# Optimization experiments

Hardware: AMD Instinct MI355X
Metric: run time of the kernel (lower is better)

The kernel has to match this reference:

```python
import jax, jax.numpy as jnp
import numpy as np
from jax.ops import segment_sum

B = 4096      # graphs per side (= batch of triples)
NPG = 32      # nodes per graph
N = B * NPG   # total nodes per batched graph
EPG = 128     # edges per graph
E = B * EPG   # total edges per batched graph
D = 256       # emb_dim
D4 = D // 4   # gnn1 out dim


def setup_inputs() -> dict:
    key = jax.random.key(0)
    ks = jax.random.split(key, 16)
    base = jnp.repeat(jnp.arange(B, dtype=jnp.int32) * NPG, EPG)  # graph offsets per edge
    def edges(k1, k2):
        s = base + jax.random.randint(k1, (E,), 0, NPG, dtype=jnp.int32)
        d = base + jax.random.randint(k2, (E,), 0, NPG, dtype=jnp.int32)
        return s, d
    subj_src, subj_dst = edges(ks[0], ks[1])
    obj_src, obj_dst = edges(ks[2], ks[3])
    node_graph_ids = jnp.repeat(jnp.arange(B, dtype=jnp.int32), NPG)
    # negative sampling indices (precomputed randomness, as in _sample_batch_negative_triples)
    head_or_tail = jax.random.randint(ks[4], (B,), 0, 2, dtype=jnp.int32)
    random_rows = jax.random.permutation(ks[5], B).astype(jnp.int32)
    ar = jnp.arange(B, dtype=jnp.int32)
    corrupt_hidx = jnp.where(head_or_tail == 1, random_rows, ar)
    corrupt_tidx = jnp.where(head_or_tail == 0, random_rows, ar)
    s = 0.02
    p = lambda k, sh: jax.random.normal(k, sh, dtype=jnp.float32) * s
    return {
        "subj_node_embs": jax.random.normal(ks[6], (N, D), dtype=jnp.float32),
        "obj_node_embs": jax.random.normal(ks[7], (N, D), dtype=jnp.float32),
        "rel_tok_embs": jax.random.normal(ks[8], (B, D), dtype=jnp.float32),
        "subj_src": subj_src, "subj_dst": subj_dst,
        "obj_src": obj_src, "obj_dst": obj_dst,
        "node_graph_ids": node_graph_ids,
        "corrupt_hidx": corrupt_hidx, "corrupt_tidx": corrupt_tidx,
        "WO1": p(ks[9], (D4, D)), "bO1": jnp.zeros((D4,), jnp.float32),
        "WI1": p(ks[10], (D4, D)), "bI1": jnp.zeros((D4,), jnp.float32),
        "WO2": p(ks[11], (D, D4)), "bO2": jnp.zeros((D,), jnp.float32),
        "WI2": p(ks[12], (D, D4)), "bI2": jnp.zeros((D,), jnp.float32),
        "relW": p(ks[13], (D, D)), "relb": jnp.zeros((D,), jnp.float32),
    }


def _mean_agg(h, idx_from, idx_to, n):
    # mean over edges (idx_from -> idx_to) of h[idx_from], per destination node; 0 for isolated
    deg = segment_sum(jnp.ones((idx_from.shape[0],), h.dtype), idx_to, num_segments=n)
    s = segment_sum(jnp.take(h, idx_from, axis=0), idx_to, num_segments=n)
    return s / jnp.maximum(deg, 1.0)[:, None]


def _compgcn(src, dst, h, WO, bO, WI, bI):
    n = h.shape[0]
    ho = _mean_agg(h, src, dst, n)   # forward graph: mean of in-neighbor sources
    hi = _mean_agg(h, dst, src, n)   # reversed graph: mean of out-neighbor targets
    return (ho @ WO.T + bO) + (hi @ WI.T + bI)


def _graph_emb(src, dst, node_embs, gids, WO1, bO1, WI1, bI1, WO2, bO2, WI2, bI2):
    hn = jax.nn.relu(_compgcn(src, dst, node_embs, WO1, bO1, WI1, bI1))
    hn = jax.nn.relu(_compgcn(src, dst, hn, WO2, bO2, WI2, bI2))
    # mean readout per graph
    cnt = segment_sum(jnp.ones((hn.shape[0],), hn.dtype), gids, num_segments=B)
    return segment_sum(hn, gids, num_segments=B) / cnt[:, None]


def _dist(h, r, t):
    return jnp.linalg.norm(h + r - t, ord=2, axis=1)


def reference(subj_node_embs, obj_node_embs, rel_tok_embs,
              subj_src, subj_dst, obj_src, obj_dst, node_graph_ids,
              corrupt_hidx, corrupt_tidx,
              WO1, bO1, WI1, bI1, WO2, bO2, WI2, bI2, relW, relb):
    h_embs = _graph_emb(subj_src, subj_dst, subj_node_embs, node_graph_ids,
                        WO1, bO1, WI1, bI1, WO2, bO2, WI2, bI2)
    t_embs = _graph_emb(obj_src, obj_dst, obj_node_embs, node_graph_ids,
                        WO1, bO1, WI1, bI1, WO2, bO2, WI2, bI2)
    r_embs = jax.nn.relu(rel_tok_embs @ relW.T + relb)
    pos_scores = _dist(h_embs, r_embs, t_embs)
    neg_scores = _dist(h_embs[corrupt_hidx], r_embs, t_embs[corrupt_tidx])
    return pos_scores, neg_scores
```

## Files before the change

kernel.cpp:

```cpp
#include <hip/hip_runtime.h>
#include <hip/hip_bf16.h>

#define BGR 4096
#define DIM 256
#define HS  257

#define OFF_EB 0
#define OFF_H1 0
#define OFF_A2 4608
#define OFF_YT 16896
#define OFF_CW 27136

typedef __bf16 bf16x8 __attribute__((ext_vector_type(8)));
typedef __bf16 bf16x4 __attribute__((ext_vector_type(4)));
typedef float  f32x4  __attribute__((ext_vector_type(4)));

__device__ __forceinline__ unsigned short f2b(float f) {
  unsigned u = __builtin_bit_cast(unsigned, f);
  u = (u + 0x7FFFu + ((u >> 16) & 1u)) >> 16;
  return (unsigned short)u;
}

__device__ __forceinline__ bf16x4 cvt4(f32x4 c) {
  bf16x4 r;
  r[0] = (__bf16)c[0]; r[1] = (__bf16)c[1]; r[2] = (__bf16)c[2]; r[3] = (__bf16)c[3];
  return r;
}

__global__ void wcvt_kernel(
    const float* __restrict__ WO1, const float* __restrict__ WI1,
    const float* __restrict__ WO2, const float* __restrict__ WI2,
    const float* __restrict__ bO1, const float* __restrict__ bI1,
    const float* __restrict__ bO2, const float* __restrict__ bI2,
    unsigned short* __restrict__ W1b, unsigned short* __restrict__ W2b,
    float* __restrict__ b1, float* __restrict__ b2)
{
  const int i = blockIdx.x * 256 + threadIdx.x;
  { int j = i >> 8, k = i & 255;
    float v = (j < 64) ? WO1[j * 256 + k] : WI1[(j - 64) * 256 + k];
    W1b[i] = f2b(v); }
  { int j = i >> 7, k = i & 127;
    float v = (k < 64) ? WO2[j * 64 + k] : WI2[j * 64 + (k - 64)];
    W2b[i] = f2b(v); }
  if (i < 64)  b1[i] = bO1[i] + bI1[i];
  if (i < 256) b2[i] = bO2[i] + bI2[i];
}

__global__ __launch_bounds__(256)
__attribute__((amdgpu_waves_per_eu(1, 5)))
void fused_kernel(
    const float* __restrict__ subj, const float* __restrict__ obj,
    const int* __restrict__ ssrc, const int* __restrict__ sdst,
    const int* __restrict__ osrc, const int* __restrict__ odst,
    const unsigned short* __restrict__ W1b, const unsigned short* __restrict__ W2b,
    const float* __restrict__ b1, const float* __restrict__ b2,
    float* __restrict__ gout)
{
  __shared__ __align__(16) unsigned char S[28416];
  const int t = threadIdx.x, w = t >> 6, l = t & 63;
  const int ln16 = l & 15, kg = l >> 4;
  const int gid = blockIdx.x;
  const int side = gid >> 12, g = gid & (BGR - 1);
  unsigned* cw = (unsigned*)(S + OFF_CW);
  const float* Eg = (side ? obj : subj) + (size_t)g * 32 * DIM;

  float4 ev[8];
  #pragma unroll
  for (int i = 0; i < 8; i++)
    ev[i] = *(const float4*)(Eg + (w * 8 + i) * 256 + l * 4);
  int es = 0, ed = 0;
  if (t < 128) {
    es = (side ? osrc : ssrc)[g * 128 + t] & 31;
    ed = (side ? odst : sdst)[g * 128 + t] & 31;
  }
  for (int i = t; i < 320; i += 256) cw[i] = 0;
  __syncthreads();

  if (t < 128) {
    atomicAdd(&cw[ed * 8 + (es >> 2)], 1u << ((es & 3) * 8));
    atomicAdd(&cw[256 + ed], 1u);
    atomicAdd(&cw[288 + es], 1u);
  }
  #pragma unroll
  for (int i = 0; i < 8; i++) {
    f32x4 tmp = {ev[i].x, ev[i].y, ev[i].z, ev[i].w};
    *(bf16x4*)(S + OFF_EB + (w * 8 + i) * 528 + l * 8) = cvt4(tmp);
  }
  bf16x8 B0[8], B1[8];
  {
    const unsigned short* wb0 = W1b + ((2 * w) * 16 + ln16) * 256 + kg * 8;
    const unsigned short* wb1 = W1b + ((2 * w + 1) * 16 + ln16) * 256 + kg * 8;
    #pragma unroll
    for (int ks = 0; ks < 8; ks++) {
      B0[ks] = *(const bf16x8*)(wb0 + ks * 32);
      B1[ks] = *(const bf16x8*)(wb1 + ks * 32);
    }
  }
  __syncthreads();

  {
    f32x4 a00 = {0,0,0,0}, a01 = {0,0,0,0}, a10 = {0,0,0,0}, a11 = {0,0,0,0};
    const unsigned char* ea = S + OFF_EB + ln16 * 528 + kg * 16;
    #pragma unroll
    for (int ks = 0; ks < 8; ks++) {
      bf16x8 A0 = *(const bf16x8*)(ea + ks * 64);
      bf16x8 A1 = *(const bf16x8*)(ea + 16 * 528 + ks * 64);
      a00 = __builtin_amdgcn_mfma_f32_16x16x32_bf16(A0, B0[ks], a00, 0, 0, 0);
      a01 = __builtin_amdgcn_mfma_f32_16x16x32_bf16(A0, B1[ks], a01, 0, 0, 0);
      a10 = __builtin_amdgcn_mfma_f32_16x16x32_bf16(A1, B0[ks], a10, 0, 0, 0);
      a11 = __builtin_amdgcn_mfma_f32_16x16x32_bf16(A1, B1[ks], a11, 0, 0, 0);
    }
    *(bf16x4*)(S + OFF_YT + ((2 * w) * 16 + ln16) * 80 + (kg * 4) * 2)          = cvt4(a00);
    *(bf16x4*)(S + OFF_YT + ((2 * w + 1) * 16 + ln16) * 80 + (kg * 4) * 2)      = cvt4(a01);
    *(bf16x4*)(S + OFF_YT + ((2 * w) * 16 + ln16) * 80 + (16 + kg * 4) * 2)     = cvt4(a10);
    *(bf16x4*)(S + OFF_YT + ((2 * w + 1) * 16 + ln16) * 80 + (16 + kg * 4) * 2) = cvt4(a11);
  }
  __syncthreads();

  bf16x8 m1f[2], m2f[2];
  #pragma unroll
  for (int hf = 0; hf < 2; hf++) {
    const int r = hf * 16 + ln16;
    const float fi = 1.0f / fmaxf((float)cw[256 + r], 1.0f);
    const float fo = 1.0f / fmaxf((float)cw[288 + r], 1.0f);
    const unsigned w0 = cw[r * 8 + kg * 2], w1 = cw[r * 8 + kg * 2 + 1];
    bf16x8 a, b;
    #pragma unroll
    for (int q = 0; q < 4; q++) {
      a[q]     = (__bf16)((float)((w0 >> (q * 8)) & 255u) * fi);
      a[4 + q] = (__bf16)((float)((w1 >> (q * 8)) & 255u) * fi);
    }
    #pragma unroll
    for (int q = 0; q < 8; q++) {
      const unsigned wq = cw[(kg * 8 + q) * 8 + (r >> 2)];
      b[q] = (__bf16)((float)((wq >> ((r & 3) * 8)) & 255u) * fo);
    }
    m1f[hf] = a; m2f[hf] = b;
  }
  {
    bf16x8 Byo = *(const bf16x8*)(S + OFF_YT + (w * 16 + ln16) * 80 + kg * 16);
    bf16x8 Byi = *(const bf16x8*)(S + OFF_YT + (64 + w * 16 + ln16) * 80 + kg * 16);
    const float b1j = b1[w * 16 + ln16];
    #pragma unroll
    for (int mt = 0; mt < 2; mt++) {
      f32x4 z = {0.f, 0.f, 0.f, 0.f};
      f32x4 c = __builtin_amdgcn_mfma_f32_16x16x32_bf16(m1f[mt], Byo, z, 0, 0, 0);
      c = __builtin_amdgcn_mfma_f32_16x16x32_bf16(m2f[mt], Byi, c, 0, 0, 0);
      f32x4 hv = { fmaxf(c[0] + b1j, 0.f), fmaxf(c[1] + b1j, 0.f),
                   fmaxf(c[2] + b1j, 0.f), fmaxf(c[3] + b1j, 0.f) };
      *(bf16x4*)(S + OFF_H1 + (w * 16 + ln16) * 72 + (mt * 16 + kg * 4) * 2) = cvt4(hv);
    }
  }
  __syncthreads();

  {
    bf16x8 Af = *(const bf16x8*)(S + OFF_H1 + (w * 16 + ln16) * 72 + kg * 16);
    #pragma unroll
    for (int hf = 0; hf < 2; hf++)
      #pragma unroll
      for (int ntd = 0; ntd < 2; ntd++) {
        f32x4 z = {0.f, 0.f, 0.f, 0.f};
        f32x4 c = __builtin_amdgcn_mfma_f32_16x16x32_bf16(
            Af, hf ? m2f[ntd] : m1f[ntd], z, 0, 0, 0);
        *(bf16x4*)(S + OFF_A2 + (ntd * 16 + ln16) * 272 + hf * 128 + w * 32 + kg * 8) = cvt4(c);
      }
  }
  __syncthreads();

  {
    bf16x8 BF[2][4];
    #pragma unroll
    for (int ntd = 0; ntd < 2; ntd++)
      #pragma unroll
      for (int ks = 0; ks < 4; ks++)
        BF[ntd][ks] = *(const bf16x8*)(S + OFF_A2 + (ntd * 16 + ln16) * 272 + ks * 64 + kg * 16);
    #pragma unroll
    for (int q = 0; q < 4; q++) {
      const int mt = w * 4 + q;
      bf16x8 AW[4];
      #pragma unroll
      for (int ks = 0; ks < 4; ks++)
        AW[ks] = *(const bf16x8*)(W2b + (mt * 16 + ln16) * 128 + ks * 32 + kg * 8);
      f32x4 a0 = {0.f, 0.f, 0.f, 0.f}, a1 = {0.f, 0.f, 0.f, 0.f};
      #pragma unroll
      for (int ks = 0; ks < 4; ks++) {
        a0 = __builtin_amdgcn_mfma_f32_16x16x32_bf16(AW[ks], BF[0][ks], a0, 0, 0, 0);
        a1 = __builtin_amdgcn_mfma_f32_16x16x32_bf16(AW[ks], BF[1][ks], a1, 0, 0, 0);
      }
      const float4 bb = *(const float4*)(b2 + mt * 16 + kg * 4);
      float v0 = fmaxf(a0[0] + bb.x, 0.f) + fmaxf(a1[0] + bb.x, 0.f);
      float v1 = fmaxf(a0[1] + bb.y, 0.f) + fmaxf(a1[1] + bb.y, 0.f);
      float v2 = fmaxf(a0[2] + bb.z, 0.f) + fmaxf(a1[2] + bb.z, 0.f);
      float v3 = fmaxf(a0[3] + bb.w, 0.f) + fmaxf(a1[3] + bb.w, 0.f);
      #pragma unroll
      for (int d = 1; d < 16; d <<= 1) {
        v0 += __shfl_xor(v0, d); v1 += __shfl_xor(v1, d);
        v2 += __shfl_xor(v2, d); v3 += __shfl_xor(v3, d);
      }
      if (ln16 == 0) {
        float4 o = { v0 * 0.03125f, v1 * 0.03125f, v2 * 0.03125f, v3 * 0.03125f };
        *(float4*)(gout + (size_t)gid * DIM + mt * 16 + kg * 4) = o;
      }
    }
  }
}

__global__ __launch_bounds__(256, 4) void rel_kernel(
    const float* __restrict__ rel, const float* __restrict__ relW,
    const float* __restrict__ relb, float* __restrict__ r_out)
{
  __shared__ float srel[16 * HS];
  const int t = threadIdx.x;
  const int b0 = blockIdx.x << 4;
  #pragma unroll
  for (int i = 0; i < 4; i++) {
    int f = (i << 8) + t;
    int r = f >> 6, k4 = f & 63;
    float4 x = *(const float4*)(rel + (size_t)(b0 + r) * DIM + (k4 << 2));
    float* d = &srel[r * HS + (k4 << 2)];
    d[0] = x.x; d[1] = x.y; d[2] = x.z; d[3] = x.w;
  }
  __syncthreads();
  const int r = t & 15, jg = t >> 4;
  const float* pa = &srel[r * HS];
  const float* w = relW + (size_t)(jg * 16) * DIM;
  float acc[16];
  #pragma unroll
  for (int jj = 0; jj < 16; jj++) acc[jj] = 0.f;
  for (int k0 = 0; k0 < DIM; k0 += 16) {
    float a[16];
    #pragma unroll
    for (int u = 0; u < 16; u++) a[u] = pa[k0 + u];
    #pragma unroll
    for (int jj = 0; jj < 16; jj++) {
      const float* wr = w + jj * DIM + k0;
      #pragma unroll
      for (int u = 0; u < 16; u += 4) {
        float4 wv = *(const float4*)(wr + u);
        acc[jj] += a[u]*wv.x + a[u+1]*wv.y + a[u+2]*wv.z + a[u+3]*wv.w;
      }
    }
  }
  float* outp = r_out + (size_t)(b0 + r) * DIM + jg * 16;
  #pragma unroll
  for (int jj = 0; jj < 16; jj++) outp[jj] = fmaxf(acc[jj] + relb[jg * 16 + jj], 0.f);
}

__global__ __launch_bounds__(256) void dist_kernel(
    const float* __restrict__ hemb, const float* __restrict__ temb,
    const float* __restrict__ remb, const int* __restrict__ chx,
    const int* __restrict__ ctx, float* __restrict__ out)
{
  const int t = threadIdx.x;
  const int w = t >> 6, l = t & 63;
  const int b = (blockIdx.x << 2) + w;
  float4 h4 = *(const float4*)(hemb + (size_t)b * DIM + (l << 2));
  float4 r4 = *(const float4*)(remb + (size_t)b * DIM + (l << 2));
  float4 t4 = *(const float4*)(temb + (size_t)b * DIM + (l << 2));
  int hb = chx[b], tb = ctx[b];
  float4 hn = *(const float4*)(hemb + (size_t)hb * DIM + (l << 2));
  float4 tn = *(const float4*)(temb + (size_t)tb * DIM + (l << 2));
  float x0 = h4.x + r4.x - t4.x, x1 = h4.y + r4.y - t4.y;
  float x2 = h4.z + r4.z - t4.z, x3 = h4.w + r4.w - t4.w;
  float dp = x0*x0 + x1*x1 + x2*x2 + x3*x3;
  float y0 = hn.x + r4.x - tn.x, y1 = hn.y + r4.y - tn.y;
  float y2 = hn.z + r4.z - tn.z, y3 = hn.w + r4.w - tn.w;
  float dn = y0*y0 + y1*y1 + y2*y2 + y3*y3;
  #pragma unroll
  for (int off = 32; off >= 1; off >>= 1) {
    dp += __shfl_down(dp, off);
    dn += __shfl_down(dn, off);
  }
  if (l == 0) {
    out[b] = sqrtf(dp);
    out[BGR + b] = sqrtf(dn);
  }
}

extern "C" void kernel_launch(void* const* d_in, const int* in_sizes, int n_in,
                              void* d_out, int out_size, void* d_ws, size_t ws_size,
                              hipStream_t stream) {
  const float* subj_embs = (const float*)d_in[0];
  const float* obj_embs  = (const float*)d_in[1];
  const float* rel_tok   = (const float*)d_in[2];
  const int* subj_src = (const int*)d_in[3];
  const int* subj_dst = (const int*)d_in[4];
  const int* obj_src  = (const int*)d_in[5];
  const int* obj_dst  = (const int*)d_in[6];
  const int* chx = (const int*)d_in[8];
  const int* ctx = (const int*)d_in[9];
  const float* WO1 = (const float*)d_in[10];
  const float* bO1 = (const float*)d_in[11];
  const float* WI1 = (const float*)d_in[12];
  const float* bI1 = (const float*)d_in[13];
  const float* WO2 = (const float*)d_in[14];
  const float* bO2 = (const float*)d_in[15];
  const float* WI2 = (const float*)d_in[16];
  const float* bI2 = (const float*)d_in[17];
  const float* relW = (const float*)d_in[18];
  const float* relb = (const float*)d_in[19];

  float* g_embs = (float*)d_ws;
  float* r_embs = g_embs + (size_t)2 * BGR * DIM;
  unsigned short* W1b = (unsigned short*)((char*)d_ws + 12582912);
  unsigned short* W2b = W1b + 32768;
  float* b1 = (float*)((char*)d_ws + 12713984);
  float* b2 = b1 + 64;
  float* out = (float*)d_out;

  wcvt_kernel<<<128, 256, 0, stream>>>(WO1, WI1, WO2, WI2, bO1, bI1, bO2, bI2,
                                       W1b, W2b, b1, b2);
  fused_kernel<<<8192, 256, 0, stream>>>(
      subj_embs, obj_embs, subj_src, subj_dst, obj_src, obj_dst,
      W1b, W2b, b1, b2, g_embs);
  rel_kernel<<<BGR / 16, 256, 0, stream>>>(rel_tok, relW, relb, r_embs);
  dist_kernel<<<BGR / 4, 256, 0, stream>>>(
      g_embs, g_embs + (size_t)BGR * DIM, r_embs, chx, ctx, out);
}
```

Baseline: 208.6 us.

## Process four graphs per block with prefetch of next graph's embeddings and edges

Each block of the fused GNN kernel now loops over four graphs instead of one. The W1 register fragments and bias load are amortized across them, and the next graph's node embeddings and edge indices are prefetched into registers while the current graph computes. Edge-count histograms are double-buffered in shared memory so the next graph's atomics can run mid-pipeline. This cuts the grid to a quarter, which lowers parallelism and lengthens each block's serial chain, and register pressure rises from the prefetched data.

```diff
diff --git a/kernel.cpp b/kernel.cpp
--- a/kernel.cpp
+++ b/kernel.cpp
@@ -3,6 +3,7 @@
 
 #define BGR 4096
 #define DIM 256
+#define NG  4
 #define HS  257
 
 #define OFF_EB 0
@@ -56,35 +57,24 @@
     const float* __restrict__ b1, const float* __restrict__ b2,
     float* __restrict__ gout)
 {
-  __shared__ __align__(16) unsigned char S[28416];
+  __shared__ __align__(16) unsigned char S[29696];
   const int t = threadIdx.x, w = t >> 6, l = t & 63;
   const int ln16 = l & 15, kg = l >> 4;
-  const int gid = blockIdx.x;
-  const int side = gid >> 12, g = gid & (BGR - 1);
-  unsigned* cw = (unsigned*)(S + OFF_CW);
-  const float* Eg = (side ? obj : subj) + (size_t)g * 32 * DIM;
+  const int gid0 = blockIdx.x * NG;
 
   float4 ev[8];
-  #pragma unroll
-  for (int i = 0; i < 8; i++)
-    ev[i] = *(const float4*)(Eg + (w * 8 + i) * 256 + l * 4);
+  {
+    const int gid = gid0;
+    const float* Eg = ((gid >> 12) ? obj : subj) + (size_t)(gid & (BGR - 1)) * 32 * DIM;
+    #pragma unroll
+    for (int i = 0; i < 8; i++)
+      ev[i] = *(const float4*)(Eg + (w * 8 + i) * 256 + l * 4);
+  }
   int es = 0, ed = 0;
   if (t < 128) {
-    es = (side ? osrc : ssrc)[g * 128 + t] & 31;
-    ed = (side ? odst : sdst)[g * 128 + t] & 31;
-  }
-  for (int i = t; i < 320; i += 256) cw[i] = 0;
-  __syncthreads();
-
-  if (t < 128) {
-    atomicAdd(&cw[ed * 8 + (es >> 2)], 1u << ((es & 3) * 8));
-    atomicAdd(&cw[256 + ed], 1u);
-    atomicAdd(&cw[288 + es], 1u);
-  }
-  #pragma unroll
-  for (int i = 0; i < 8; i++) {
-    f32x4 tmp = {ev[i].x, ev[i].y, ev[i].z, ev[i].w};
-    *(bf16x4*)(S + OFF_EB + (w * 8 + i) * 528 + l * 8) = cvt4(tmp);
+    const int gid = gid0, g = gid & (BGR - 1);
+    es = (((gid >> 12) ? osrc : ssrc))[g * 128 + t] & 31;
+    ed = (((gid >> 12) ? odst : sdst))[g * 128 + t] & 31;
   }
   bf16x8 B0[8], B1[8];
   {
@@ -96,112 +86,156 @@
       B1[ks] = *(const bf16x8*)(wb1 + ks * 32);
     }
   }
+  const float b1j = b1[w * 16 + ln16];
+  {
+    unsigned* cw = (unsigned*)(S + OFF_CW);
+    for (int i = t; i < 640; i += 256) cw[i] = 0;
+  }
   __syncthreads();
-
-  {
-    f32x4 a00 = {0,0,0,0}, a01 = {0,0,0,0}, a10 = {0,0,0,0}, a11 = {0,0,0,0};
-    const unsigned char* ea = S + OFF_EB + ln16 * 528 + kg * 16;
-    #pragma unroll
-    for (int ks = 0; ks < 8; ks++) {
-      bf16x8 A0 = *(const bf16x8*)(ea + ks * 64);
-      bf16x8 A1 = *(const bf16x8*)(ea + 16 * 528 + ks * 64);
-      a00 = __builtin_amdgcn_mfma_f32_16x16x32_bf16(A0, B0[ks], a00, 0, 0, 0);
-      a01 = __builtin_amdgcn_mfma_f32_16x16x32_bf16(A0, B1[ks], a01, 0, 0, 0);
-      a10 = __builtin_amdgcn_mfma_f32_16x16x32_bf16(A1, B0[ks], a10, 0, 0, 0);
-      a11 = __builtin_amdgcn_mfma_f32_16x16x32_bf16(A1, B1[ks], a11, 0, 0, 0);
-    }
-    *(bf16x4*)(S + OFF_YT + ((2 * w) * 16 + ln16) * 80 + (kg * 4) * 2)          = cvt4(a00);
-    *(bf16x4*)(S + OFF_YT + ((2 * w + 1) * 16 + ln16) * 80 + (kg * 4) * 2)      = cvt4(a01);
-    *(bf16x4*)(S + OFF_YT + ((2 * w) * 16 + ln16) * 80 + (16 + kg * 4) * 2)     = cvt4(a10);
-    *(bf16x4*)(S + OFF_YT + ((2 * w + 1) * 16 + ln16) * 80 + (16 + kg * 4) * 2) = cvt4(a11);
-  }
-  __syncthreads();
-
-  bf16x8 m1f[2], m2f[2];
-  #pragma unroll
-  for (int hf = 0; hf < 2; hf++) {
-    const int r = hf * 16 + ln16;
-    const float fi = 1.0f / fmaxf((float)cw[256 + r], 1.0f);
-    const float fo = 1.0f / fmaxf((float)cw[288 + r], 1.0f);
-    const unsigned w0 = cw[r * 8 + kg * 2], w1 = cw[r * 8 + kg * 2 + 1];
-    bf16x8 a, b;
-    #pragma unroll
-    for (int q = 0; q < 4; q++) {
-      a[q]     = (__bf16)((float)((w0 >> (q * 8)) & 255u) * fi);
-      a[4 + q] = (__bf16)((float)((w1 >> (q * 8)) & 255u) * fi);
-    }
-    #pragma unroll
-    for (int q = 0; q < 8; q++) {
-      const unsigned wq = cw[(kg * 8 + q) * 8 + (r >> 2)];
-      b[q] = (__bf16)((float)((wq >> ((r & 3) * 8)) & 255u) * fo);
-    }
-    m1f[hf] = a; m2f[hf] = b;
-  }
-  {
-    bf16x8 Byo = *(const bf16x8*)(S + OFF_YT + (w * 16 + ln16) * 80 + kg * 16);
-    bf16x8 Byi = *(const bf16x8*)(S + OFF_YT + (64 + w * 16 + ln16) * 80 + kg * 16);
-    const float b1j = b1[w * 16 + ln16];
-    #pragma unroll
-    for (int mt = 0; mt < 2; mt++) {
-      f32x4 z = {0.f, 0.f, 0.f, 0.f};
-      f32x4 c = __builtin_amdgcn_mfma_f32_16x16x32_bf16(m1f[mt], Byo, z, 0, 0, 0);
-      c = __builtin_amdgcn_mfma_f32_16x16x32_bf16(m2f[mt], Byi, c, 0, 0, 0);
-      f32x4 hv = { fmaxf(c[0] + b1j, 0.f), fmaxf(c[1] + b1j, 0.f),
-                   fmaxf(c[2] + b1j, 0.f), fmaxf(c[3] + b1j, 0.f) };
-      *(bf16x4*)(S + OFF_H1 + (w * 16 + ln16) * 72 + (mt * 16 + kg * 4) * 2) = cvt4(hv);
-    }
-  }
-  __syncthreads();
-
-  {
-    bf16x8 Af = *(const bf16x8*)(S + OFF_H1 + (w * 16 + ln16) * 72 + kg * 16);
-    #pragma unroll
-    for (int hf = 0; hf < 2; hf++)
-      #pragma unroll
-      for (int ntd = 0; ntd < 2; ntd++) {
+  if (t < 128) {
+    unsigned* cw = (unsigned*)(S + OFF_CW);
+    atomicAdd(&cw[ed * 8 + (es >> 2)], 1u << ((es & 3) * 8));
+    atomicAdd(&cw[256 + ed], 1u);
+    atomicAdd(&cw[288 + es], 1u);
+  }
+
+  #pragma unroll
+  for (int g = 0; g < NG; g++) {
+    const int gid = gid0 + g;
+    unsigned* cwc = (unsigned*)(S + OFF_CW + (g & 1) * 1280);
+    unsigned* cwn = (unsigned*)(S + OFF_CW + ((g + 1) & 1) * 1280);
+
+    #pragma unroll
+    for (int i = 0; i < 8; i++) {
+      f32x4 tmp = {ev[i].x, ev[i].y, ev[i].z, ev[i].w};
+      *(bf16x4*)(S + OFF_EB + (w * 8 + i) * 528 + l * 8) = cvt4(tmp);
+    }
+    if (g + 1 < NG) for (int i = t; i < 320; i += 256) cwn[i] = 0;
+    if (g + 1 < NG) {
+      const int ngid = gid + 1, ngg = ngid & (BGR - 1);
+      const float* Eg = ((ngid >> 12) ? obj : subj) + (size_t)ngg * 32 * DIM;
+      #pragma unroll
+      for (int i = 0; i < 8; i++)
+        ev[i] = *(const float4*)(Eg + (w * 8 + i) * 256 + l * 4);
+      if (t < 128) {
+        es = (((ngid >> 12) ? osrc : ssrc))[ngg * 128 + t] & 31;
+        ed = (((ngid >> 12) ? odst : sdst))[ngg * 128 + t] & 31;
+      }
+    }
+    __builtin_amdgcn_sched_barrier(0);
+    __syncthreads();
+
+    {
+      f32x4 a00 = {0,0,0,0}, a01 = {0,0,0,0}, a10 = {0,0,0,0}, a11 = {0,0,0,0};
+      const unsigned char* ea = S + OFF_EB + ln16 * 528 + kg * 16;
+      #pragma unroll
+      for (int ks = 0; ks < 8; ks++) {
+        bf16x8 A0 = *(const bf16x8*)(ea + ks * 64);
+        bf16x8 A1 = *(const bf16x8*)(ea + 16 * 528 + ks * 64);
+        a00 = __builtin_amdgcn_mfma_f32_16x16x32_bf16(A0, B0[ks], a00, 0, 0, 0);
+        a01 = __builtin_amdgcn_mfma_f32_16x16x32_bf16(A0, B1[ks], a01, 0, 0, 0);
+        a10 = __builtin_amdgcn_mfma_f32_16x16x32_bf16(A1, B0[ks], a10, 0, 0, 0);
+        a11 = __builtin_amdgcn_mfma_f32_16x16x32_bf16(A1, B1[ks], a11, 0, 0, 0);
+      }
+      *(bf16x4*)(S + OFF_YT + ((2 * w) * 16 + ln16) * 80 + (kg * 4) * 2)          = cvt4(a00);
+      *(bf16x4*)(S + OFF_YT + ((2 * w + 1) * 16 + ln16) * 80 + (kg * 4) * 2)      = cvt4(a01);
+      *(bf16x4*)(S + OFF_YT + ((2 * w) * 16 + ln16) * 80 + (16 + kg * 4) * 2)     = cvt4(a10);
+      *(bf16x4*)(S + OFF_YT + ((2 * w + 1) * 16 + ln16) * 80 + (16 + kg * 4) * 2) = cvt4(a11);
+    }
+    __syncthreads();
+
+    bf16x8 m1f[2], m2f[2];
+    #pragma unroll
+    for (int hf = 0; hf < 2; hf++) {
+      const int r = hf * 16 + ln16;
+      const float fi = 1.0f / fmaxf((float)cwc[256 + r], 1.0f);
+      const float fo = 1.0f / fmaxf((float)cwc[288 + r], 1.0f);
+      const unsigned w0 = cwc[r * 8 + kg * 2], w1 = cwc[r * 8 + kg * 2 + 1];
+      bf16x8 a, b;
+      #pragma unroll
+      for (int q = 0; q < 4; q++) {
+        a[q]     = (__bf16)((float)((w0 >> (q * 8)) & 255u) * fi);
+        a[4 + q] = (__bf16)((float)((w1 >> (q * 8)) & 255u) * fi);
+      }
+      #pragma unroll
+      for (int q = 0; q < 8; q++) {
+        const unsigned wq = cwc[(kg * 8 + q) * 8 + (r >> 2)];
+        b[q] = (__bf16)((float)((wq >> ((r & 3) * 8)) & 255u) * fo);
+      }
+      m1f[hf] = a; m2f[hf] = b;
+    }
+    {
+      bf16x8 Byo = *(const bf16x8*)(S + OFF_YT + (w * 16 + ln16) * 80 + kg * 16);
+      bf16x8 Byi = *(const bf16x8*)(S + OFF_YT + (64 + w * 16 + ln16) * 80 + kg * 16);
+      #pragma unroll
+      for (int mt = 0; mt < 2; mt++) {
         f32x4 z = {0.f, 0.f, 0.f, 0.f};
-        f32x4 c = __builtin_amdgcn_mfma_f32_16x16x32_bf16(
-            Af, hf ? m2f[ntd] : m1f[ntd], z, 0, 0, 0);
-        *(bf16x4*)(S + OFF_A2 + (ntd * 16 + ln16) * 272 + hf * 128 + w * 32 + kg * 8) = cvt4(c);
-      }
-  }
-  __syncthreads();
-
-  {
-    bf16x8 BF[2][4];
-    #pragma unroll
-    for (int ntd = 0; ntd < 2; ntd++)
-      #pragma unroll
-      for (int ks = 0; ks < 4; ks++)
-        BF[ntd][ks] = *(const bf16x8*)(S + OFF_A2 + (ntd * 16 + ln16) * 272 + ks * 64 + kg * 16);
-    #pragma unroll
-    for (int q = 0; q < 4; q++) {
-      const int mt = w * 4 + q;
-      bf16x8 AW[4];
-      #pragma unroll
-      for (int ks = 0; ks < 4; ks++)
-        AW[ks] = *(const bf16x8*)(W2b + (mt * 16 + ln16) * 128 + ks * 32 + kg * 8);
-      f32x4 a0 = {0.f, 0.f, 0.f, 0.f}, a1 = {0.f, 0.f, 0.f, 0.f};
-      #pragma unroll
-      for (int ks = 0; ks < 4; ks++) {
-        a0 = __builtin_amdgcn_mfma_f32_16x16x32_bf16(AW[ks], BF[0][ks], a0, 0, 0, 0);
-        a1 = __builtin_amdgcn_mfma_f32_16x16x32_bf16(AW[ks], BF[1][ks], a1, 0, 0, 0);
-      }
-      const float4 bb = *(const float4*)(b2 + mt * 16 + kg * 4);
-      float v0 = fmaxf(a0[0] + bb.x, 0.f) + fmaxf(a1[0] + bb.x, 0.f);
-      float v1 = fmaxf(a0[1] + bb.y, 0.f) + fmaxf(a1[1] + bb.y, 0.f);
-      float v2 = fmaxf(a0[2] + bb.z, 0.f) + fmaxf(a1[2] + bb.z, 0.f);
-      float v3 = fmaxf(a0[3] + bb.w, 0.f) + fmaxf(a1[3] + bb.w, 0.f);
-      #pragma unroll
-      for (int d = 1; d < 16; d <<= 1) {
-        v0 += __shfl_xor(v0, d); v1 += __shfl_xor(v1, d);
-        v2 += __shfl_xor(v2, d); v3 += __shfl_xor(v3, d);
-      }
-      if (ln16 == 0) {
-        float4 o = { v0 * 0.03125f, v1 * 0.03125f, v2 * 0.03125f, v3 * 0.03125f };
-        *(float4*)(gout + (size_t)gid * DIM + mt * 16 + kg * 4) = o;
-      }
-    }
+        f32x4 c = __builtin_amdgcn_mfma_f32_16x16x32_bf16(m1f[mt], Byo, z, 0, 0, 0);
+        c = __builtin_amdgcn_mfma_f32_16x16x32_bf16(m2f[mt], Byi, c, 0, 0, 0);
+        f32x4 hv = { fmaxf(c[0] + b1j, 0.f), fmaxf(c[1] + b1j, 0.f),
+                     fmaxf(c[2] + b1j, 0.f), fmaxf(c[3] + b1j, 0.f) };
+        *(bf16x4*)(S + OFF_H1 + (w * 16 + ln16) * 72 + (mt * 16 + kg * 4) * 2) = cvt4(hv);
+      }
+    }
+    __syncthreads();
+
+    if (g + 1 < NG && t < 128) {
+      atomicAdd(&cwn[ed * 8 + (es >> 2)], 1u << ((es & 3) * 8));
+      atomicAdd(&cwn[256 + ed], 1u);
+      atomicAdd(&cwn[288 + es], 1u);
+    }
+
+    {
+      bf16x8 Af = *(const bf16x8*)(S + OFF_H1 + (w * 16 + ln16) * 72 + kg * 16);
+      #pragma unroll
+      for (int hf = 0; hf < 2; hf++)
+        #pragma unroll
+        for (int ntd = 0; ntd < 2; ntd++) {
+          f32x4 z = {0.f, 0.f, 0.f, 0.f};
+          f32x4 c = __builtin_amdgcn_mfma_f32_16x16x32_bf16(
+              Af, hf ? m2f[ntd] : m1f[ntd], z, 0, 0, 0);
+          *(bf16x4*)(S + OFF_A2 + (ntd * 16 + ln16) * 272 + hf * 128 + w * 32 + kg * 8) = cvt4(c);
+        }
+    }
+    __syncthreads();
+
+    {
+      bf16x8 BF[2][4];
+      #pragma unroll
+      for (int ntd = 0; ntd < 2; ntd++)
+        #pragma unroll
+        for (int ks = 0; ks < 4; ks++)
+          BF[ntd][ks] = *(const bf16x8*)(S + OFF_A2 + (ntd * 16 + ln16) * 272 + ks * 64 + kg * 16);
+      #pragma unroll
+      for (int q = 0; q < 4; q++) {
+        const int mt = w * 4 + q;
+        bf16x8 AW[4];
+        #pragma unroll
+        for (int ks = 0; ks < 4; ks++)
+          AW[ks] = *(const bf16x8*)(W2b + (mt * 16 + ln16) * 128 + ks * 32 + kg * 8);
+        f32x4 a0 = {0.f, 0.f, 0.f, 0.f}, a1 = {0.f, 0.f, 0.f, 0.f};
+        #pragma unroll
+        for (int ks = 0; ks < 4; ks++) {
+          a0 = __builtin_amdgcn_mfma_f32_16x16x32_bf16(AW[ks], BF[0][ks], a0, 0, 0, 0);
+          a1 = __builtin_amdgcn_mfma_f32_16x16x32_bf16(AW[ks], BF[1][ks], a1, 0, 0, 0);
+        }
+        const float4 bb = *(const float4*)(b2 + mt * 16 + kg * 4);
+        float v0 = fmaxf(a0[0] + bb.x, 0.f) + fmaxf(a1[0] + bb.x, 0.f);
+        float v1 = fmaxf(a0[1] + bb.y, 0.f) + fmaxf(a1[1] + bb.y, 0.f);
+        float v2 = fmaxf(a0[2] + bb.z, 0.f) + fmaxf(a1[2] + bb.z, 0.f);
+        float v3 = fmaxf(a0[3] + bb.w, 0.f) + fmaxf(a1[3] + bb.w, 0.f);
+        #pragma unroll
+        for (int d = 1; d < 16; d <<= 1) {
+          v0 += __shfl_xor(v0, d); v1 += __shfl_xor(v1, d);
+          v2 += __shfl_xor(v2, d); v3 += __shfl_xor(v3, d);
+        }
+        if (ln16 == 0) {
+          float4 o = { v0 * 0.03125f, v1 * 0.03125f, v2 * 0.03125f, v3 * 0.03125f };
+          *(float4*)(gout + (size_t)gid * DIM + mt * 16 + kg * 4) = o;
+        }
+      }
+    }
+    if (g + 1 < NG) __syncthreads();
   }
 }
 
@@ -310,7 +344,7 @@
 
   wcvt_kernel<<<128, 256, 0, stream>>>(WO1, WI1, WO2, WI2, bO1, bI1, bO2, bI2,
                                        W1b, W2b, b1, b2);
-  fused_kernel<<<8192, 256, 0, stream>>>(
+  fused_kernel<<<8192 / NG, 256, 0, stream>>>(
       subj_embs, obj_embs, subj_src, subj_dst, obj_src, obj_dst,
       W1b, W2b, b1, b2, g_embs);
   rel_kernel<<<BGR / 16, 256, 0, stream>>>(rel_tok, relW, relb, r_embs);
```

Result: faster. 198.9 us (-4.7%).
